# Kernel optimization log

Measured on AMD Instinct MI355X. Metric: run time of the kernel, lower is better.

## Reference

```python
import jax, jax.numpy as jnp
import numpy as np

N = 8192      # n_nodes == nfeat (square feature matrix, required by final Linear)
NHID = 64
NCLASS = 8
E = N * 32    # avg degree 32


def setup_inputs() -> dict:
    key = jax.random.key(0)
    ks = jax.random.split(key, 12)
    s = 1.0 / np.sqrt(NHID)
    return {
        "x": jax.random.normal(ks[0], (N, N), dtype=jnp.float32),
        "adj_row": jax.random.randint(ks[1], (E,), 0, N, dtype=jnp.int32),
        "adj_col": jax.random.randint(ks[2], (E,), 0, N, dtype=jnp.int32),
        "adj_val": jax.random.uniform(ks[3], (E,), dtype=jnp.float32),
        "W1": jax.random.uniform(ks[4], (N, NHID), minval=-s, maxval=s, dtype=jnp.float32),
        "b1": jax.random.uniform(ks[5], (NHID,), minval=-s, maxval=s, dtype=jnp.float32),
        "W2": jax.random.uniform(ks[6], (NHID, NHID), minval=-s, maxval=s, dtype=jnp.float32),
        "b2": jax.random.uniform(ks[7], (NHID,), minval=-s, maxval=s, dtype=jnp.float32),
        "W3": jax.random.uniform(ks[8], (NHID, NCLASS), minval=-s, maxval=s, dtype=jnp.float32),
        "b3": jax.random.uniform(ks[9], (NCLASS,), minval=-s, maxval=s, dtype=jnp.float32),
        "Wlin": jax.random.normal(ks[10], (1, N), dtype=jnp.float32) * (1.0 / np.sqrt(N)),
        "blin": jax.random.normal(ks[11], (1,), dtype=jnp.float32) * 0.01,
    }


def _gcn_layer(h, W, b, row, col, val):
    # support = h @ W ; out = spmm(adj, support) + b
    support = h @ W                              # [N, F_out]
    msgs = val[:, None] * support[col]           # gather source rows, scale by edge value
    out = jax.ops.segment_sum(msgs, row, num_segments=N)  # scatter-add into dest rows
    return out + b


def reference(x, adj_row, adj_col, adj_val, W1, b1, W2, b2, W3, b3, Wlin, blin):
    h = jax.nn.relu(_gcn_layer(x, W1, b1, adj_row, adj_col, adj_val))
    # dropout inactive (eval mode)
    h = jax.nn.relu(_gcn_layer(h, W2, b2, adj_row, adj_col, adj_val))
    h = _gcn_layer(h, W3, b3, adj_row, adj_col, adj_val)   # [N, NCLASS]
    h = jax.nn.log_softmax(h, axis=1)
    # LinearLayer(nfeat->1) applied to h^T [NCLASS, N] -> [NCLASS, 1], then transpose
    y = h.T @ Wlin.T + blin                      # [NCLASS, 1]
    return y.T                                   # [1, NCLASS]
```

## Files before the change

kernel.cpp:

```cpp
#include <hip/hip_runtime.h>

#define NN 8192
#define NHID 64
#define NCLASS 8
#define NEDGE (NN * 32)

typedef __attribute__((ext_vector_type(8))) short bf16x8_t;
typedef __attribute__((ext_vector_type(4))) float f32x4_t;

__device__ __forceinline__ unsigned short f2bf(float f) {
    unsigned int u = __float_as_uint(f);
    u += 0x7FFF + ((u >> 16) & 1);
    return (unsigned short)(u >> 16);
}

__global__ __launch_bounds__(256) void w1t_kernel(const float* __restrict__ W1,
                                                  unsigned short* __restrict__ w1t) {
    const int idx = blockIdx.x * 256 + threadIdx.x;
    const int n = idx >> 13;
    const int k = idx & (NN - 1);
    w1t[idx] = f2bf(W1[(size_t)k * NHID + n]);
}

__global__ __launch_bounds__(256) void hist_kernel(const int* __restrict__ row,
                                                   int* __restrict__ counts) {
    const int e = blockIdx.x * 256 + threadIdx.x;
    if (e < NEDGE) atomicAdd(&counts[row[e]], 1);
}

__global__ __launch_bounds__(1024) void scan_kernel(const int* __restrict__ counts,
                                                    int* __restrict__ row_start,
                                                    int* __restrict__ row_fill) {
    __shared__ int sdata[1024];
    const int tid = threadIdx.x;
    int loc[8];
    int t = 0;
#pragma unroll
    for (int j = 0; j < 8; ++j) { loc[j] = counts[tid * 8 + j]; t += loc[j]; }
    sdata[tid] = t;
    __syncthreads();
    for (int off = 1; off < 1024; off <<= 1) {
        const int add = (tid >= off) ? sdata[tid - off] : 0;
        __syncthreads();
        sdata[tid] += add;
        __syncthreads();
    }
    int excl = sdata[tid] - t;
#pragma unroll
    for (int j = 0; j < 8; ++j) {
        row_start[tid * 8 + j] = excl;
        row_fill[tid * 8 + j] = excl;
        excl += loc[j];
    }
    if (tid == 1023) row_start[NN] = excl;
}

__global__ __launch_bounds__(256) void scatter_kernel(const int* __restrict__ row,
                                                      const int* __restrict__ col,
                                                      const float* __restrict__ val,
                                                      int* __restrict__ row_fill,
                                                      int* __restrict__ ccol,
                                                      float* __restrict__ cval) {
    const int e = blockIdx.x * 256 + threadIdx.x;
    if (e >= NEDGE) return;
    const int pos = atomicAdd(&row_fill[row[e]], 1);
    ccol[pos] = col[e];
    cval[pos] = val[e];
}

__global__ __launch_bounds__(256, 2) void gemm1_kernel(const float* __restrict__ x,
                                                       const unsigned short* __restrict__ w1t,
                                                       float* __restrict__ outp) {
    __shared__ short As[128][72];
    __shared__ short Bs[64][72];
    const int tid = threadIdx.x;
    const int r0 = blockIdx.x * 128;
    const int k0base = blockIdx.y * (NN / 8);
    const int lane = tid & 63;
    const int wv = tid >> 6;
    const int m16 = lane & 15;
    const int quad = lane >> 4;
    const int c4 = tid & 15;
    const int rA = tid >> 4;

    f32x4_t acc[2][4];
#pragma unroll
    for (int i = 0; i < 2; ++i)
#pragma unroll
        for (int j = 0; j < 4; ++j) acc[i][j] = (f32x4_t){0.f, 0.f, 0.f, 0.f};

    for (int kt = 0; kt < (NN / 8) / 64; ++kt) {
        const int k0 = k0base + kt * 64;
#pragma unroll
        for (int i = 0; i < 8; ++i) {
            const int r = rA + i * 16;
            const float4 v = *(const float4*)(x + (size_t)(r0 + r) * NN + k0 + c4 * 4);
            *(ushort4*)(&As[r][c4 * 4]) =
                make_ushort4(f2bf(v.x), f2bf(v.y), f2bf(v.z), f2bf(v.w));
        }
#pragma unroll
        for (int it = 0; it < 2; ++it) {
            const int idx = tid + it * 256;
            const int n = idx >> 3;
            const int kc = idx & 7;
            *(uint4*)(&Bs[n][kc * 8]) = *(const uint4*)(w1t + (size_t)n * NN + k0 + kc * 8);
        }
        __syncthreads();
#pragma unroll
        for (int kk = 0; kk < 64; kk += 32) {
            bf16x8_t af[2], bfr[4];
#pragma unroll
            for (int rt = 0; rt < 2; ++rt)
                af[rt] = *(const bf16x8_t*)(&As[wv * 32 + rt * 16 + m16][kk + quad * 8]);
#pragma unroll
            for (int ct = 0; ct < 4; ++ct)
                bfr[ct] = *(const bf16x8_t*)(&Bs[ct * 16 + m16][kk + quad * 8]);
#pragma unroll
            for (int rt = 0; rt < 2; ++rt)
#pragma unroll
                for (int ct = 0; ct < 4; ++ct)
                    acc[rt][ct] = __builtin_amdgcn_mfma_f32_16x16x32_bf16(
                        af[rt], bfr[ct], acc[rt][ct], 0, 0, 0);
        }
        __syncthreads();
    }
#pragma unroll
    for (int rt = 0; rt < 2; ++rt)
#pragma unroll
        for (int ct = 0; ct < 4; ++ct)
#pragma unroll
            for (int reg = 0; reg < 4; ++reg) {
                const int row = r0 + wv * 32 + rt * 16 + quad * 4 + reg;
                const int col = ct * 16 + m16;
                atomicAdd(&outp[(size_t)row * NHID + col], acc[rt][ct][reg]);
            }
}

__global__ __launch_bounds__(256) void spmm64_kernel(const float* __restrict__ sup,
                                                     const int* __restrict__ row_start,
                                                     const int* __restrict__ ccol,
                                                     const float* __restrict__ cval,
                                                     const float* __restrict__ bias,
                                                     float* __restrict__ outp,
                                                     const int do_relu) {
    const int wid = (blockIdx.x * 256 + threadIdx.x) >> 6;
    const int lane = threadIdx.x & 63;
    const int s = row_start[wid];
    const int e = row_start[wid + 1];
    float acc = 0.f;
    for (int i = s; i < e; ++i) {
        const int c = ccol[i];
        const float v = cval[i];
        acc = fmaf(v, sup[(size_t)c * NHID + lane], acc);
    }
    acc += bias[lane];
    if (do_relu) acc = fmaxf(acc, 0.f);
    outp[(size_t)wid * NHID + lane] = acc;
}

__global__ __launch_bounds__(256) void spmm8_kernel(const float* __restrict__ sup,
                                                    const int* __restrict__ row_start,
                                                    const int* __restrict__ ccol,
                                                    const float* __restrict__ cval,
                                                    const float* __restrict__ bias,
                                                    float* __restrict__ outp) {
    const int gid = blockIdx.x * 256 + threadIdx.x;
    const int r = gid >> 3;
    const int c = gid & 7;
    const int s = row_start[r];
    const int e = row_start[r + 1];
    float acc = 0.f;
    for (int i = s; i < e; ++i)
        acc = fmaf(cval[i], sup[(size_t)ccol[i] * NCLASS + c], acc);
    outp[(size_t)r * NCLASS + c] = acc + bias[c];
}

__global__ __launch_bounds__(256) void gemm2_kernel(const float* __restrict__ h,
                                                    const float* __restrict__ W,
                                                    float* __restrict__ outp) {
    __shared__ float Ws[NHID * NHID];
    for (int i = threadIdx.x; i < NHID * NHID; i += 256) Ws[i] = W[i];
    __syncthreads();
    const int lane = threadIdx.x & 63;
    const int wv = threadIdx.x >> 6;
    const int rbase = blockIdx.x * 32 + wv * 8;
    for (int rr = 0; rr < 8; ++rr) {
        const int r = rbase + rr;
        const float hval = h[(size_t)r * NHID + lane];
        float acc = 0.f;
#pragma unroll
        for (int k = 0; k < NHID; ++k)
            acc = fmaf(__shfl(hval, k, 64), Ws[k * NHID + lane], acc);
        outp[(size_t)r * NHID + lane] = acc;
    }
}

__global__ __launch_bounds__(256) void gemm3_kernel(const float* __restrict__ h,
                                                    const float* __restrict__ W,
                                                    float* __restrict__ outp) {
    __shared__ float Ws[NHID * NCLASS];
    for (int i = threadIdx.x; i < NHID * NCLASS; i += 256) Ws[i] = W[i];
    __syncthreads();
    const int gid = blockIdx.x * 256 + threadIdx.x;
    const int r = gid >> 3;
    const int c = gid & 7;
    const float* hr = h + (size_t)r * NHID;
    float acc = 0.f;
#pragma unroll
    for (int k4 = 0; k4 < NHID / 4; ++k4) {
        const float4 hv = *(const float4*)(hr + k4 * 4);
        acc = fmaf(hv.x, Ws[(k4 * 4 + 0) * NCLASS + c], acc);
        acc = fmaf(hv.y, Ws[(k4 * 4 + 1) * NCLASS + c], acc);
        acc = fmaf(hv.z, Ws[(k4 * 4 + 2) * NCLASS + c], acc);
        acc = fmaf(hv.w, Ws[(k4 * 4 + 3) * NCLASS + c], acc);
    }
    outp[(size_t)r * NCLASS + c] = acc;
}

__global__ __launch_bounds__(256) void lsm_kernel(float* __restrict__ h) {
    const int r = blockIdx.x * 256 + threadIdx.x;
    float4 a = *(float4*)(h + (size_t)r * 8);
    float4 b = *(float4*)(h + (size_t)r * 8 + 4);
    const float m = fmaxf(fmaxf(fmaxf(a.x, a.y), fmaxf(a.z, a.w)),
                          fmaxf(fmaxf(b.x, b.y), fmaxf(b.z, b.w)));
    const float s = expf(a.x - m) + expf(a.y - m) + expf(a.z - m) + expf(a.w - m) +
                    expf(b.x - m) + expf(b.y - m) + expf(b.z - m) + expf(b.w - m);
    const float lse = m + logf(s);
    a.x -= lse; a.y -= lse; a.z -= lse; a.w -= lse;
    b.x -= lse; b.y -= lse; b.z -= lse; b.w -= lse;
    *(float4*)(h + (size_t)r * 8) = a;
    *(float4*)(h + (size_t)r * 8 + 4) = b;
}

__global__ void init_out_kernel(float* __restrict__ outp, const float* __restrict__ blin) {
    if (threadIdx.x < NCLASS) outp[threadIdx.x] = blin[0];
}

__global__ __launch_bounds__(256) void final_kernel(const float* __restrict__ ls,
                                                    const float* __restrict__ wlin,
                                                    float* __restrict__ outp) {
    const int gid = blockIdx.x * 256 + threadIdx.x;
    const float w = wlin[gid];
    const float4 a = *(const float4*)(ls + (size_t)gid * 8);
    const float4 b = *(const float4*)(ls + (size_t)gid * 8 + 4);
    float p[8] = {a.x * w, a.y * w, a.z * w, a.w * w,
                  b.x * w, b.y * w, b.z * w, b.w * w};
#pragma unroll
    for (int off = 32; off > 0; off >>= 1) {
#pragma unroll
        for (int c = 0; c < 8; ++c) p[c] += __shfl_down(p[c], off);
    }
    if ((threadIdx.x & 63) == 0) {
#pragma unroll
        for (int c = 0; c < 8; ++c) atomicAdd(&outp[c], p[c]);
    }
}

extern "C" void kernel_launch(void* const* d_in, const int* in_sizes, int n_in,
                              void* d_out, int out_size, void* d_ws, size_t ws_size,
                              hipStream_t stream) {
    const float* x       = (const float*)d_in[0];
    const int*   adj_row = (const int*)d_in[1];
    const int*   adj_col = (const int*)d_in[2];
    const float* adj_val = (const float*)d_in[3];
    const float* W1      = (const float*)d_in[4];
    const float* b1      = (const float*)d_in[5];
    const float* W2      = (const float*)d_in[6];
    const float* b2      = (const float*)d_in[7];
    const float* W3      = (const float*)d_in[8];
    const float* b3      = (const float*)d_in[9];
    const float* Wlin    = (const float*)d_in[10];
    const float* blin    = (const float*)d_in[11];
    float* outp = (float*)d_out;

    char* ws = (char*)d_ws;
    float*          bufA      = (float*)ws;
    float*          bufB      = (float*)(ws + (2u << 20));
    unsigned short* w1t       = (unsigned short*)(ws + (4u << 20));
    int*            ccol      = (int*)(ws + (5u << 20));
    float*          cval      = (float*)(ws + (6u << 20));
    int*            row_start = (int*)(ws + (7u << 20));
    int*            row_fill  = (int*)(ws + (7u << 20) + (64u << 10));
    int*            counts    = (int*)(ws + (7u << 20) + (128u << 10));

    hipMemsetAsync(bufA, 0, (size_t)NN * NHID * sizeof(float), stream);
    hipMemsetAsync(counts, 0, (size_t)NN * sizeof(int), stream);

    init_out_kernel<<<1, 64, 0, stream>>>(outp, blin);
    w1t_kernel<<<(NHID * NN) / 256, 256, 0, stream>>>(W1, w1t);
    hist_kernel<<<NEDGE / 256, 256, 0, stream>>>(adj_row, counts);
    scan_kernel<<<1, 1024, 0, stream>>>(counts, row_start, row_fill);
    scatter_kernel<<<NEDGE / 256, 256, 0, stream>>>(adj_row, adj_col, adj_val,
                                                    row_fill, ccol, cval);
    gemm1_kernel<<<dim3(NN / 128, 8), 256, 0, stream>>>(x, w1t, bufA);
    spmm64_kernel<<<(NN * 64) / 256, 256, 0, stream>>>(bufA, row_start, ccol, cval, b1, bufB, 1);
    gemm2_kernel<<<NN / 32, 256, 0, stream>>>(bufB, W2, bufA);
    spmm64_kernel<<<(NN * 64) / 256, 256, 0, stream>>>(bufA, row_start, ccol, cval, b2, bufB, 1);
    gemm3_kernel<<<(NN * 8) / 256, 256, 0, stream>>>(bufB, W3, bufA);
    spmm8_kernel<<<(NN * 8) / 256, 256, 0, stream>>>(bufA, row_start, ccol, cval, b3, bufB);
    lsm_kernel<<<NN / 256, 256, 0, stream>>>(bufB);
    final_kernel<<<NN / 256, 256, 0, stream>>>(bufB, Wlin, outp);
}
```

Baseline: 553.9 us.

## Fuse GCN layers into fewer kernels and replace gemm1 atomics with split-K reduce

Fuses the dense layer-2 and layer-3 transforms into the preceding SpMM kernels. It also merges log-softmax and the final linear reduction into the last SpMM, and combines the W1 transpose with the histogram pass. gemm1 now writes per-split partials and a separate reduce kernel sums them, instead of issuing float atomicAdds into a memset buffer. This cuts kernel launches and intermediate round trips through global memory. In exchange it needs a much larger workspace and extra partial-buffer traffic, and each SpMM-A block now loads W2 into shared memory.

```diff
diff --git a/kernel.cpp b/kernel.cpp
--- a/kernel.cpp
+++ b/kernel.cpp
@@ -4,6 +4,7 @@
 #define NHID 64
 #define NCLASS 8
 #define NEDGE (NN * 32)
+#define NSPLIT 8
 
 typedef __attribute__((ext_vector_type(8))) short bf16x8_t;
 typedef __attribute__((ext_vector_type(4))) float f32x4_t;
@@ -14,18 +15,20 @@
     return (unsigned short)(u >> 16);
 }
 
-__global__ __launch_bounds__(256) void w1t_kernel(const float* __restrict__ W1,
-                                                  unsigned short* __restrict__ w1t) {
-    const int idx = blockIdx.x * 256 + threadIdx.x;
-    const int n = idx >> 13;
-    const int k = idx & (NN - 1);
-    w1t[idx] = f2bf(W1[(size_t)k * NHID + n]);
-}
-
-__global__ __launch_bounds__(256) void hist_kernel(const int* __restrict__ row,
+__global__ __launch_bounds__(256) void prep_kernel(const float* __restrict__ W1,
+                                                   unsigned short* __restrict__ w1t,
+                                                   const int* __restrict__ row,
                                                    int* __restrict__ counts) {
-    const int e = blockIdx.x * 256 + threadIdx.x;
-    if (e < NEDGE) atomicAdd(&counts[row[e]], 1);
+    const int bid = blockIdx.x;
+    if (bid < 2048) {
+        const int idx = bid * 256 + threadIdx.x;
+        const int n = idx >> 13;
+        const int k = idx & (NN - 1);
+        w1t[idx] = f2bf(W1[(size_t)k * NHID + n]);
+    } else {
+        const int e = (bid - 2048) * 256 + threadIdx.x;
+        atomicAdd(&counts[row[e]], 1);
+    }
 }
 
 __global__ __launch_bounds__(1024) void scan_kernel(const int* __restrict__ counts,
@@ -70,12 +73,12 @@
 
 __global__ __launch_bounds__(256, 2) void gemm1_kernel(const float* __restrict__ x,
                                                        const unsigned short* __restrict__ w1t,
-                                                       float* __restrict__ outp) {
+                                                       float* __restrict__ part) {
     __shared__ short As[128][72];
     __shared__ short Bs[64][72];
     const int tid = threadIdx.x;
     const int r0 = blockIdx.x * 128;
-    const int k0base = blockIdx.y * (NN / 8);
+    const int k0base = blockIdx.y * (NN / NSPLIT);
     const int lane = tid & 63;
     const int wv = tid >> 6;
     const int m16 = lane & 15;
@@ -89,7 +92,7 @@
 #pragma unroll
         for (int j = 0; j < 4; ++j) acc[i][j] = (f32x4_t){0.f, 0.f, 0.f, 0.f};
 
-    for (int kt = 0; kt < (NN / 8) / 64; ++kt) {
+    for (int kt = 0; kt < (NN / NSPLIT) / 64; ++kt) {
         const int k0 = k0base + kt * 64;
 #pragma unroll
         for (int i = 0; i < 8; ++i) {
@@ -124,6 +127,7 @@
         }
         __syncthreads();
     }
+    float* op = part + (size_t)blockIdx.y * (NN * NHID);
 #pragma unroll
     for (int rt = 0; rt < 2; ++rt)
 #pragma unroll
@@ -132,38 +136,88 @@
             for (int reg = 0; reg < 4; ++reg) {
                 const int row = r0 + wv * 32 + rt * 16 + quad * 4 + reg;
                 const int col = ct * 16 + m16;
-                atomicAdd(&outp[(size_t)row * NHID + col], acc[rt][ct][reg]);
+                op[(size_t)row * NHID + col] = acc[rt][ct][reg];
             }
 }
 
-__global__ __launch_bounds__(256) void spmm64_kernel(const float* __restrict__ sup,
-                                                     const int* __restrict__ row_start,
-                                                     const int* __restrict__ ccol,
-                                                     const float* __restrict__ cval,
-                                                     const float* __restrict__ bias,
-                                                     float* __restrict__ outp,
-                                                     const int do_relu) {
+__global__ __launch_bounds__(256) void reduce8_kernel(const float* __restrict__ part,
+                                                      float* __restrict__ sup) {
+    const int i = blockIdx.x * 256 + threadIdx.x;
+    const float4* p4 = (const float4*)part;
+    float4 a = p4[i];
+#pragma unroll
+    for (int s = 1; s < NSPLIT; ++s) {
+        const float4 b = p4[i + (size_t)s * (NN * NHID / 4)];
+        a.x += b.x; a.y += b.y; a.z += b.z; a.w += b.w;
+    }
+    ((float4*)sup)[i] = a;
+}
+
+__global__ __launch_bounds__(256) void spmmA_kernel(const float* __restrict__ sup,
+                                                    const int* __restrict__ row_start,
+                                                    const int* __restrict__ ccol,
+                                                    const float* __restrict__ cval,
+                                                    const float* __restrict__ b1,
+                                                    const float* __restrict__ W2,
+                                                    float* __restrict__ s2out) {
+    __shared__ float Ws[NHID * NHID];
+    for (int i = threadIdx.x; i < NHID * NHID; i += 256) Ws[i] = W2[i];
+    __syncthreads();
     const int wid = (blockIdx.x * 256 + threadIdx.x) >> 6;
     const int lane = threadIdx.x & 63;
     const int s = row_start[wid];
     const int e = row_start[wid + 1];
     float acc = 0.f;
-    for (int i = s; i < e; ++i) {
-        const int c = ccol[i];
-        const float v = cval[i];
-        acc = fmaf(v, sup[(size_t)c * NHID + lane], acc);
-    }
-    acc += bias[lane];
-    if (do_relu) acc = fmaxf(acc, 0.f);
-    outp[(size_t)wid * NHID + lane] = acc;
-}
-
-__global__ __launch_bounds__(256) void spmm8_kernel(const float* __restrict__ sup,
+    for (int i = s; i < e; ++i)
+        acc = fmaf(cval[i], sup[(size_t)ccol[i] * NHID + lane], acc);
+    acc = fmaxf(acc + b1[lane], 0.f);
+    float o = 0.f;
+#pragma unroll
+    for (int k = 0; k < NHID; ++k)
+        o = fmaf(__shfl(acc, k, 64), Ws[k * NHID + lane], o);
+    s2out[(size_t)wid * NHID + lane] = o;
+}
+
+__global__ __launch_bounds__(256) void spmmB_kernel(const float* __restrict__ s2,
                                                     const int* __restrict__ row_start,
                                                     const int* __restrict__ ccol,
                                                     const float* __restrict__ cval,
-                                                    const float* __restrict__ bias,
-                                                    float* __restrict__ outp) {
+                                                    const float* __restrict__ b2,
+                                                    const float* __restrict__ W3,
+                                                    float* __restrict__ s3out) {
+    const int wid = (blockIdx.x * 256 + threadIdx.x) >> 6;
+    const int lane = threadIdx.x & 63;
+    const float4 w3a = *(const float4*)(W3 + lane * NCLASS);
+    const float4 w3b = *(const float4*)(W3 + lane * NCLASS + 4);
+    const int s = row_start[wid];
+    const int e = row_start[wid + 1];
+    float acc = 0.f;
+    for (int i = s; i < e; ++i)
+        acc = fmaf(cval[i], s2[(size_t)ccol[i] * NHID + lane], acc);
+    acc = fmaxf(acc + b2[lane], 0.f);
+    float p[8] = {acc * w3a.x, acc * w3a.y, acc * w3a.z, acc * w3a.w,
+                  acc * w3b.x, acc * w3b.y, acc * w3b.z, acc * w3b.w};
+#pragma unroll
+    for (int off = 32; off > 0; off >>= 1)
+#pragma unroll
+        for (int c = 0; c < 8; ++c) p[c] += __shfl_down(p[c], off, 64);
+    if (lane == 0) {
+        float4 r0 = {p[0], p[1], p[2], p[3]};
+        float4 r1 = {p[4], p[5], p[6], p[7]};
+        *(float4*)(s3out + (size_t)wid * NCLASS) = r0;
+        *(float4*)(s3out + (size_t)wid * NCLASS + 4) = r1;
+    }
+}
+
+__global__ __launch_bounds__(256) void tail_kernel(const float* __restrict__ s3,
+                                                   const int* __restrict__ row_start,
+                                                   const int* __restrict__ ccol,
+                                                   const float* __restrict__ cval,
+                                                   const float* __restrict__ b3,
+                                                   const float* __restrict__ wlin,
+                                                   const float* __restrict__ blin,
+                                                   float* __restrict__ outp) {
+    __shared__ float cls[4 * NCLASS];
     const int gid = blockIdx.x * 256 + threadIdx.x;
     const int r = gid >> 3;
     const int c = gid & 7;
@@ -171,88 +225,29 @@
     const int e = row_start[r + 1];
     float acc = 0.f;
     for (int i = s; i < e; ++i)
-        acc = fmaf(cval[i], sup[(size_t)ccol[i] * NCLASS + c], acc);
-    outp[(size_t)r * NCLASS + c] = acc + bias[c];
-}
-
-__global__ __launch_bounds__(256) void gemm2_kernel(const float* __restrict__ h,
-                                                    const float* __restrict__ W,
-                                                    float* __restrict__ outp) {
-    __shared__ float Ws[NHID * NHID];
-    for (int i = threadIdx.x; i < NHID * NHID; i += 256) Ws[i] = W[i];
+        acc = fmaf(cval[i], s3[(size_t)ccol[i] * NCLASS + c], acc);
+    acc += b3[c];
+    float m = acc;
+    m = fmaxf(m, __shfl_xor(m, 1, 8));
+    m = fmaxf(m, __shfl_xor(m, 2, 8));
+    m = fmaxf(m, __shfl_xor(m, 4, 8));
+    float sx = expf(acc - m);
+    sx += __shfl_xor(sx, 1, 8);
+    sx += __shfl_xor(sx, 2, 8);
+    sx += __shfl_xor(sx, 4, 8);
+    const float ls = acc - m - logf(sx);
+    float p = ls * wlin[r];
+    p += __shfl_xor(p, 8, 64);
+    p += __shfl_xor(p, 16, 64);
+    p += __shfl_xor(p, 32, 64);
+    const int wv = threadIdx.x >> 6;
+    if ((threadIdx.x & 63) < 8) cls[wv * NCLASS + c] = p;
     __syncthreads();
-    const int lane = threadIdx.x & 63;
-    const int wv = threadIdx.x >> 6;
-    const int rbase = blockIdx.x * 32 + wv * 8;
-    for (int rr = 0; rr < 8; ++rr) {
-        const int r = rbase + rr;
-        const float hval = h[(size_t)r * NHID + lane];
-        float acc = 0.f;
-#pragma unroll
-        for (int k = 0; k < NHID; ++k)
-            acc = fmaf(__shfl(hval, k, 64), Ws[k * NHID + lane], acc);
-        outp[(size_t)r * NHID + lane] = acc;
-    }
-}
-
-__global__ __launch_bounds__(256) void gemm3_kernel(const float* __restrict__ h,
-                                                    const float* __restrict__ W,
-                                                    float* __restrict__ outp) {
-    __shared__ float Ws[NHID * NCLASS];
-    for (int i = threadIdx.x; i < NHID * NCLASS; i += 256) Ws[i] = W[i];
-    __syncthreads();
-    const int gid = blockIdx.x * 256 + threadIdx.x;
-    const int r = gid >> 3;
-    const int c = gid & 7;
-    const float* hr = h + (size_t)r * NHID;
-    float acc = 0.f;
-#pragma unroll
-    for (int k4 = 0; k4 < NHID / 4; ++k4) {
-        const float4 hv = *(const float4*)(hr + k4 * 4);
-        acc = fmaf(hv.x, Ws[(k4 * 4 + 0) * NCLASS + c], acc);
-        acc = fmaf(hv.y, Ws[(k4 * 4 + 1) * NCLASS + c], acc);
-        acc = fmaf(hv.z, Ws[(k4 * 4 + 2) * NCLASS + c], acc);
-        acc = fmaf(hv.w, Ws[(k4 * 4 + 3) * NCLASS + c], acc);
-    }
-    outp[(size_t)r * NCLASS + c] = acc;
-}
-
-__global__ __launch_bounds__(256) void lsm_kernel(float* __restrict__ h) {
-    const int r = blockIdx.x * 256 + threadIdx.x;
-    float4 a = *(float4*)(h + (size_t)r * 8);
-    float4 b = *(float4*)(h + (size_t)r * 8 + 4);
-    const float m = fmaxf(fmaxf(fmaxf(a.x, a.y), fmaxf(a.z, a.w)),
-                          fmaxf(fmaxf(b.x, b.y), fmaxf(b.z, b.w)));
-    const float s = expf(a.x - m) + expf(a.y - m) + expf(a.z - m) + expf(a.w - m) +
-                    expf(b.x - m) + expf(b.y - m) + expf(b.z - m) + expf(b.w - m);
-    const float lse = m + logf(s);
-    a.x -= lse; a.y -= lse; a.z -= lse; a.w -= lse;
-    b.x -= lse; b.y -= lse; b.z -= lse; b.w -= lse;
-    *(float4*)(h + (size_t)r * 8) = a;
-    *(float4*)(h + (size_t)r * 8 + 4) = b;
-}
-
-__global__ void init_out_kernel(float* __restrict__ outp, const float* __restrict__ blin) {
-    if (threadIdx.x < NCLASS) outp[threadIdx.x] = blin[0];
-}
-
-__global__ __launch_bounds__(256) void final_kernel(const float* __restrict__ ls,
-                                                    const float* __restrict__ wlin,
-                                                    float* __restrict__ outp) {
-    const int gid = blockIdx.x * 256 + threadIdx.x;
-    const float w = wlin[gid];
-    const float4 a = *(const float4*)(ls + (size_t)gid * 8);
-    const float4 b = *(const float4*)(ls + (size_t)gid * 8 + 4);
-    float p[8] = {a.x * w, a.y * w, a.z * w, a.w * w,
-                  b.x * w, b.y * w, b.z * w, b.w * w};
-#pragma unroll
-    for (int off = 32; off > 0; off >>= 1) {
-#pragma unroll
-        for (int c = 0; c < 8; ++c) p[c] += __shfl_down(p[c], off);
-    }
-    if ((threadIdx.x & 63) == 0) {
-#pragma unroll
-        for (int c = 0; c < 8; ++c) atomicAdd(&outp[c], p[c]);
+    if (threadIdx.x < NCLASS) {
+        float v = cls[threadIdx.x] + cls[NCLASS + threadIdx.x] +
+                  cls[2 * NCLASS + threadIdx.x] + cls[3 * NCLASS + threadIdx.x];
+        if (blockIdx.x == 0) v += blin[0];
+        atomicAdd(&outp[threadIdx.x], v);
     }
 }
 
@@ -274,30 +269,28 @@
     float* outp = (float*)d_out;
 
     char* ws = (char*)d_ws;
-    float*          bufA      = (float*)ws;
-    float*          bufB      = (float*)(ws + (2u << 20));
-    unsigned short* w1t       = (unsigned short*)(ws + (4u << 20));
-    int*            ccol      = (int*)(ws + (5u << 20));
-    float*          cval      = (float*)(ws + (6u << 20));
-    int*            row_start = (int*)(ws + (7u << 20));
-    int*            row_fill  = (int*)(ws + (7u << 20) + (64u << 10));
-    int*            counts    = (int*)(ws + (7u << 20) + (128u << 10));
-
-    hipMemsetAsync(bufA, 0, (size_t)NN * NHID * sizeof(float), stream);
+    float*          part      = (float*)ws;
+    float*          sup       = (float*)(ws + (16u << 20));
+    float*          s2        = (float*)(ws + (18u << 20));
+    float*          s3        = (float*)(ws + (20u << 20));
+    unsigned short* w1t       = (unsigned short*)(ws + (21u << 20));
+    int*            ccol      = (int*)(ws + (22u << 20));
+    float*          cval      = (float*)(ws + (23u << 20));
+    int*            row_start = (int*)(ws + (24u << 20));
+    int*            row_fill  = (int*)(ws + (24u << 20) + (64u << 10));
+    int*            counts    = (int*)(ws + (24u << 20) + (128u << 10));
+
     hipMemsetAsync(counts, 0, (size_t)NN * sizeof(int), stream);
-
-    init_out_kernel<<<1, 64, 0, stream>>>(outp, blin);
-    w1t_kernel<<<(NHID * NN) / 256, 256, 0, stream>>>(W1, w1t);
-    hist_kernel<<<NEDGE / 256, 256, 0, stream>>>(adj_row, counts);
+    hipMemsetAsync(outp, 0, NCLASS * sizeof(float), stream);
+
+    prep_kernel<<<3072, 256, 0, stream>>>(W1, w1t, adj_row, counts);
     scan_kernel<<<1, 1024, 0, stream>>>(counts, row_start, row_fill);
     scatter_kernel<<<NEDGE / 256, 256, 0, stream>>>(adj_row, adj_col, adj_val,
                                                     row_fill, ccol, cval);
-    gemm1_kernel<<<dim3(NN / 128, 8), 256, 0, stream>>>(x, w1t, bufA);
-    spmm64_kernel<<<(NN * 64) / 256, 256, 0, stream>>>(bufA, row_start, ccol, cval, b1, bufB, 1);
-    gemm2_kernel<<<NN / 32, 256, 0, stream>>>(bufB, W2, bufA);
-    spmm64_kernel<<<(NN * 64) / 256, 256, 0, stream>>>(bufA, row_start, ccol, cval, b2, bufB, 1);
-    gemm3_kernel<<<(NN * 8) / 256, 256, 0, stream>>>(bufB, W3, bufA);
-    spmm8_kernel<<<(NN * 8) / 256, 256, 0, stream>>>(bufA, row_start, ccol, cval, b3, bufB);
-    lsm_kernel<<<NN / 256, 256, 0, stream>>>(bufB);
-    final_kernel<<<NN / 256, 256, 0, stream>>>(bufB, Wlin, outp);
-}
+    gemm1_kernel<<<dim3(NN / 128, NSPLIT), 256, 0, stream>>>(x, w1t, part);
+    reduce8_kernel<<<(NN * NHID / 4) / 256, 256, 0, stream>>>(part, sup);
+    spmmA_kernel<<<(NN * 64) / 256, 256, 0, stream>>>(sup, row_start, ccol, cval, b1, W2, s2);
+    spmmB_kernel<<<(NN * 64) / 256, 256, 0, stream>>>(s2, row_start, ccol, cval, b2, W3, s3);
+    tail_kernel<<<(NN * 8) / 256, 256, 0, stream>>>(s3, row_start, ccol, cval, b3,
+                                                    Wlin, blin, outp);
+}
```

Result: faster. 524.1 us (-5.4%).
